# Performance work log

Hardware: AMD Instinct MI355X
Metric: run time of the kernel (lower is better)

Reference implementation:

```python
import jax, jax.numpy as jnp
import numpy as np

D = 1024      # d_model
H = 16        # query heads
KV = 4        # kv heads
HD = D // H   # head dim = 64
REP = H // KV
E = 16        # experts
K = 2         # experts per token
INTER = 1408  # moe intermediate size
EPS = 1e-6
B, S = 2, 1024


def rmsnorm(x, w):
    return x * jax.lax.rsqrt(jnp.mean(x * x, axis=-1, keepdims=True) + EPS) * w


def rotate_half(x):
    x1, x2 = jnp.split(x, 2, axis=-1)
    return jnp.concatenate([-x2, x1], axis=-1)


def setup_inputs() -> dict:
    key = jax.random.key(0)
    ks = jax.random.split(key, 12)
    x = jax.random.normal(ks[0], (B, S, D), jnp.float32)
    # RoPE tables [S, HD]
    inv = 1.0 / (10000.0 ** (np.arange(0, HD, 2, dtype=np.float64) / HD))
    ang = np.arange(S, dtype=np.float64)[:, None] * inv[None, :]
    ang = np.concatenate([ang, ang], axis=1)
    cos = jnp.asarray(np.cos(ang), jnp.float32)
    sin = jnp.asarray(np.sin(ang), jnp.float32)
    w = lambda k, shape: jax.random.normal(k, shape, jnp.float32) * 0.02
    return dict(
        x=x, cos=cos, sin=sin,
        ln1_w=jnp.ones((D,), jnp.float32),
        wq=w(ks[1], (D, H * HD)),
        wk=w(ks[2], (D, KV * HD)),
        wv=w(ks[3], (D, KV * HD)),
        wo=w(ks[4], (H * HD, D)),
        qn_w=jnp.ones((HD,), jnp.float32),
        kn_w=jnp.ones((HD,), jnp.float32),
        ln2_w=jnp.ones((D,), jnp.float32),
        router_w=w(ks[5], (D, E)),
        w_gate=w(ks[6], (E, D, INTER)),
        w_up=w(ks[7], (E, D, INTER)),
        w_down=w(ks[8], (E, INTER, D)),
    )


def reference(x, cos, sin, ln1_w, wq, wk, wv, wo, qn_w, kn_w, ln2_w,
              router_w, w_gate, w_up, w_down):
    b, s, _ = x.shape
    # --- GQA attention with qk RMSNorm + RoPE, causal ---
    h = rmsnorm(x, ln1_w)
    q = (h @ wq).reshape(b, s, H, HD)
    k = (h @ wk).reshape(b, s, KV, HD)
    v = (h @ wv).reshape(b, s, KV, HD)
    q = rmsnorm(q, qn_w)
    k = rmsnorm(k, kn_w)
    c = cos[None, :, None, :]
    sn = sin[None, :, None, :]
    q = q * c + rotate_half(q) * sn
    k = k * c + rotate_half(k) * sn
    k = jnp.repeat(k, REP, axis=2)  # [b,s,H,HD]
    v = jnp.repeat(v, REP, axis=2)
    scores = jnp.einsum('bqhd,bkhd->bhqk', q, k) / jnp.sqrt(jnp.float32(HD))
    causal = jnp.tril(jnp.ones((s, s), bool))
    scores = jnp.where(causal[None, None], scores, jnp.finfo(scores.dtype).min)
    p = jax.nn.softmax(scores, axis=-1)
    attn = jnp.einsum('bhqk,bkhd->bqhd', p, v).reshape(b, s, H * HD) @ wo
    x = x + attn
    # --- Sparse MoE FFN (top-k softmax router, normalized top-k probs, SwiGLU experts) ---
    t = rmsnorm(x, ln2_w).reshape(b * s, D)
    logits = t @ router_w                       # [T,E]
    probs = jax.nn.softmax(logits, axis=-1)
    top_v, top_i = jax.lax.top_k(probs, K)      # [T,K]
    top_v = top_v / jnp.sum(top_v, axis=-1, keepdims=True)
    onehot = jax.nn.one_hot(top_i, E, dtype=t.dtype)      # [T,K,E]
    w_dense = jnp.einsum('tke,tk->te', onehot, top_v)     # [T,E] combine weights
    g = jnp.einsum('td,edi->eti', t, w_gate)
    u = jnp.einsum('td,edi->eti', t, w_up)
    eo = jnp.einsum('eti,eid->etd', jax.nn.silu(g) * u, w_down)
    moe = jnp.einsum('te,etd->td', w_dense, eo).reshape(b, s, D)
    # load-balancing aux loss: E * sum_e f_e * P_e
    f = jnp.mean(onehot, axis=(0, 1))           # fraction of assignments per expert
    aux = jnp.float32(E) * jnp.sum(f * jnp.mean(probs, axis=0))
    return x + moe, aux
```

## Files before the change

kernel.cpp:

```cpp
#include <hip/hip_runtime.h>

#define BB 2
#define SS 1024
#define DD 1024
#define HH 16
#define KVH 4
#define HDD 64
#define EE 16
#define II 1408
#define TT (BB*SS)
#define EPS_ 1e-6f

typedef unsigned short u16;
typedef __bf16 bf16x8 __attribute__((ext_vector_type(8)));
typedef _Float16 f16x8 __attribute__((ext_vector_type(8)));
typedef float f32x4 __attribute__((ext_vector_type(4)));

__device__ __forceinline__ float wred_sum(float v) {
#pragma unroll
  for (int o = 32; o > 0; o >>= 1) v += __shfl_xor(v, o);
  return v;
}

__device__ __forceinline__ u16 f2b(float f) {
  __bf16 h = (__bf16)f;
  return __builtin_bit_cast(u16, h);
}

__device__ __forceinline__ bf16x8 ld_frag(const u16* p) {
  return __builtin_bit_cast(bf16x8, *(const uint4*)p);
}
__device__ __forceinline__ f16x8 ldh(const u16* p) {
  return __builtin_bit_cast(f16x8, *(const uint4*)p);
}

__device__ __forceinline__ void split2h(float v, u16* o0, u16* o1) {
  _Float16 a = (_Float16)v;
  float fa = (float)a;
  _Float16 b = (_Float16)((v - fa) * 2048.0f);
  *o0 = __builtin_bit_cast(u16, a);
  *o1 = __builtin_bit_cast(u16, b);
}

#define CVAL(fm, nf, r) (accm[fm][nf][r] + accx[fm][nf][r] * 4.8828125e-4f)

__global__ __launch_bounds__(256) void k_rmsnorm_split2(const float* __restrict__ x,
    const float* __restrict__ w, u16* __restrict__ o0, u16* __restrict__ o1) {
  int row = blockIdx.x, tid = threadIdx.x;
  float4 v = ((const float4*)(x + (size_t)row * DD))[tid];
  float ss = v.x*v.x + v.y*v.y + v.z*v.z + v.w*v.w;
  ss = wred_sum(ss);
  __shared__ float red[4];
  if ((tid & 63) == 0) red[tid >> 6] = ss;
  __syncthreads();
  float tot = red[0] + red[1] + red[2] + red[3];
  float sc = rsqrtf(tot * (1.0f / DD) + EPS_);
  float4 wv = ((const float4*)w)[tid];
  float vals[4] = {v.x*sc*wv.x, v.y*sc*wv.y, v.z*sc*wv.z, v.w*sc*wv.w};
  ushort4 s0, s1;
  split2h(vals[0], &s0.x, &s1.x);
  split2h(vals[1], &s0.y, &s1.y);
  split2h(vals[2], &s0.z, &s1.z);
  split2h(vals[3], &s0.w, &s1.w);
  size_t base = (size_t)row * DD + tid * 4;
  *(ushort4*)&o0[base] = s0;
  *(ushort4*)&o1[base] = s1;
}

__global__ __launch_bounds__(256) void k_transpose_split2(const float* __restrict__ Wm,
    u16* __restrict__ T0, u16* __restrict__ T1, int K, int N) {
  int n0 = blockIdx.x * 64, k0 = blockIdx.y * 64;
  __shared__ float tile[64][65];
  int tc = threadIdx.x & 15, tr = threadIdx.x >> 4;
#pragma unroll
  for (int kk = 0; kk < 64; kk += 16) {
    float4 v = *(const float4*)&Wm[(size_t)(k0 + kk + tr) * N + n0 + tc * 4];
    tile[kk + tr][tc*4+0] = v.x; tile[kk + tr][tc*4+1] = v.y;
    tile[kk + tr][tc*4+2] = v.z; tile[kk + tr][tc*4+3] = v.w;
  }
  __syncthreads();
#pragma unroll
  for (int nn = 0; nn < 64; nn += 16) {
    int n = nn + tr;
    ushort4 s0, s1;
    split2h(tile[tc*4+0][n], &s0.x, &s1.x);
    split2h(tile[tc*4+1][n], &s0.y, &s1.y);
    split2h(tile[tc*4+2][n], &s0.z, &s1.z);
    split2h(tile[tc*4+3][n], &s0.w, &s1.w);
    size_t base = (size_t)(n0 + n) * K + k0 + tc * 4;
    *(ushort4*)&T0[base] = s0;
    *(ushort4*)&T1[base] = s1;
  }
}

#define S2GEMM_BODY(a0p, a1p, b0p, b1p, KTOT) \
  __shared__ __align__(16) u16 A0s[128][56], A1s[128][56]; \
  __shared__ __align__(16) u16 B0s[64][56], B1s[64][56]; \
  int tid = threadIdx.x, lane = tid & 63, w = tid >> 6; \
  int wm = (w & 1) * 64, wn = (w >> 1) * 32; \
  int lr = lane & 15, lk = (lane >> 4) * 8; \
  int br = tid >> 2, bc = (tid & 3) * 8; \
  f32x4 accm[4][2] = {}, accx[4][2] = {}; \
  for (int k0 = 0; k0 < (KTOT); k0 += 32) { \
    uint4 a0v0 = *(const uint4*)((a0p) + (size_t)br * (KTOT) + k0 + bc); \
    uint4 a0v1 = *(const uint4*)((a0p) + (size_t)(64 + br) * (KTOT) + k0 + bc); \
    uint4 a1v0 = *(const uint4*)((a1p) + (size_t)br * (KTOT) + k0 + bc); \
    uint4 a1v1 = *(const uint4*)((a1p) + (size_t)(64 + br) * (KTOT) + k0 + bc); \
    uint4 b0v = *(const uint4*)((b0p) + (size_t)br * (KTOT) + k0 + bc); \
    uint4 b1v = *(const uint4*)((b1p) + (size_t)br * (KTOT) + k0 + bc); \
    __syncthreads(); \
    *(uint4*)&A0s[br][bc] = a0v0; \
    *(uint4*)&A0s[64 + br][bc] = a0v1; \
    *(uint4*)&A1s[br][bc] = a1v0; \
    *(uint4*)&A1s[64 + br][bc] = a1v1; \
    *(uint4*)&B0s[br][bc] = b0v; \
    *(uint4*)&B1s[br][bc] = b1v; \
    __syncthreads(); \
    f16x8 bq0[2], bq1[2]; \
    _Pragma("unroll") \
    for (int nf = 0; nf < 2; ++nf) { \
      bq0[nf] = ldh(&B0s[wn + nf*16 + lr][lk]); \
      bq1[nf] = ldh(&B1s[wn + nf*16 + lr][lk]); } \
    _Pragma("unroll") \
    for (int fm = 0; fm < 4; ++fm) { \
      f16x8 a0 = ldh(&A0s[wm + fm*16 + lr][lk]); \
      f16x8 a1 = ldh(&A1s[wm + fm*16 + lr][lk]); \
      _Pragma("unroll") \
      for (int nf = 0; nf < 2; ++nf) { \
        accm[fm][nf] = __builtin_amdgcn_mfma_f32_16x16x32_f16(a0, bq0[nf], accm[fm][nf], 0, 0, 0); \
        f32x4 cx = accx[fm][nf]; \
        cx = __builtin_amdgcn_mfma_f32_16x16x32_f16(a0, bq1[nf], cx, 0, 0, 0); \
        cx = __builtin_amdgcn_mfma_f32_16x16x32_f16(a1, bq0[nf], cx, 0, 0, 0); \
        accx[fm][nf] = cx; } } \
  }

__global__ __launch_bounds__(256) void k_qkv_s2(
    const u16* __restrict__ h0, const u16* __restrict__ h1,
    const u16* __restrict__ wqt0, const u16* __restrict__ wqt1,
    const u16* __restrict__ wkt0, const u16* __restrict__ wkt1,
    const u16* __restrict__ wvt0, const u16* __restrict__ wvt1,
    float* __restrict__ qb, float* __restrict__ kb, float* __restrict__ vb) {
  int nt = blockIdx.x, m0 = blockIdx.y * 128;
  const u16 *B0, *B1; float* Cm; int Nm, n0;
  if (nt < 16)      { B0 = wqt0; B1 = wqt1; Cm = qb; Nm = 1024; n0 = nt * 64; }
  else if (nt < 20) { B0 = wkt0; B1 = wkt1; Cm = kb; Nm = 256;  n0 = (nt - 16) * 64; }
  else              { B0 = wvt0; B1 = wvt1; Cm = vb; Nm = 256;  n0 = (nt - 20) * 64; }
  const u16* a0p = h0 + (size_t)m0 * 1024;
  const u16* a1p = h1 + (size_t)m0 * 1024;
  const u16* b0p = B0 + (size_t)n0 * 1024;
  const u16* b1p = B1 + (size_t)n0 * 1024;
  S2GEMM_BODY(a0p, a1p, b0p, b1p, 1024)
#pragma unroll
  for (int fm = 0; fm < 4; ++fm)
#pragma unroll
    for (int nf = 0; nf < 2; ++nf)
#pragma unroll
      for (int r = 0; r < 4; ++r) {
        int row = m0 + wm + fm*16 + (lane >> 4) * 4 + r;
        Cm[(size_t)row * Nm + n0 + wn + nf*16 + lr] = CVAL(fm, nf, r);
      }
}

__global__ __launch_bounds__(256) void k_qknorm_rope_split2(
    const float* __restrict__ qb, const float* __restrict__ kb,
    const float* __restrict__ qnw, const float* __restrict__ knw,
    const float* __restrict__ cosb, const float* __restrict__ sinb,
    u16* __restrict__ q0a, u16* __restrict__ q1a,
    u16* __restrict__ k0a, u16* __restrict__ k1a) {
  int tok = blockIdx.x, grp = blockIdx.y;
  int wv = threadIdx.x >> 6, d = threadIdx.x & 63;
  int s = tok & (SS - 1);
  const float* ptr; const float* wn;
  if (grp < 4) { ptr = qb + (size_t)tok * 1024 + (grp * 4 + wv) * 64; wn = qnw; }
  else         { ptr = kb + (size_t)tok * 256 + wv * 64;              wn = knw; }
  float v = ptr[d];
  float ssum = wred_sum(v * v);
  float rms = rsqrtf(ssum * (1.0f / 64.0f) + EPS_);
  float nv = v * rms * wn[d];
  float pn = __shfl_xor(nv, 32);
  float rot = (d < 32) ? -pn : pn;
  float val = nv * cosb[s * 64 + d] + rot * sinb[s * 64 + d];
  u16 a, b;
  split2h(val, &a, &b);
  if (grp < 4) {
    size_t idx = (size_t)tok * 1024 + (grp * 4 + wv) * 64 + d;
    q0a[idx] = a; q1a[idx] = b;
  } else {
    size_t idx = (size_t)tok * 256 + wv * 64 + d;
    k0a[idx] = a; k1a[idx] = b;
  }
}

__global__ __launch_bounds__(256) void k_splitv2(const float* __restrict__ vb,
    u16* __restrict__ t0, u16* __restrict__ t1) {
  int k0 = blockIdx.x * 64, bkv = blockIdx.y;
  int b = bkv >> 2, kv = bkv & 3;
  __shared__ float tile[64][65];
  int tc = threadIdx.x & 15, tr = threadIdx.x >> 4;
#pragma unroll
  for (int kk = 0; kk < 64; kk += 16) {
    float4 v = *(const float4*)&vb[(size_t)(b * 1024 + k0 + kk + tr) * 256 + kv * 64 + tc * 4];
    tile[kk + tr][tc*4+0] = v.x; tile[kk + tr][tc*4+1] = v.y;
    tile[kk + tr][tc*4+2] = v.z; tile[kk + tr][tc*4+3] = v.w;
  }
  __syncthreads();
#pragma unroll
  for (int dd = 0; dd < 64; dd += 16) {
    int d = dd + tr;
    ushort4 s0, s1;
    split2h(tile[tc*4+0][d], &s0.x, &s1.x);
    split2h(tile[tc*4+1][d], &s0.y, &s1.y);
    split2h(tile[tc*4+2][d], &s0.z, &s1.z);
    split2h(tile[tc*4+3][d], &s0.w, &s1.w);
    size_t base = (size_t)(bkv * 64 + d) * 1024 + k0 + tc * 4;
    *(ushort4*)&t0[base] = s0;
    *(ushort4*)&t1[base] = s1;
  }
}

__global__ __launch_bounds__(256) void k_flash(
    const u16* __restrict__ qs0, const u16* __restrict__ qs1,
    const u16* __restrict__ ks0, const u16* __restrict__ ks1,
    const u16* __restrict__ vt0, const u16* __restrict__ vt1,
    u16* __restrict__ at0, u16* __restrict__ at1) {
  int pair = blockIdx.x, bh = blockIdx.y;
  int b = bh >> 4, hh = bh & 15, kv = hh >> 2;
  int bkv = b * 4 + kv;
  __shared__ __align__(16) u16 Qs0[64*72], Qs1[64*72];
  __shared__ __align__(16) u16 Ks0[64*72], Ks1[64*72];
  __shared__ __align__(16) u16 Vs0[64*72], Vs1[64*72];
  __shared__ __align__(16) u16 Ps0[64*72], Ps1[64*72];
  int tid = threadIdx.x, lane = tid & 63, w = tid >> 6;
  int lr = lane & 15, g = lane >> 4;
  int wq0 = w * 16;
  const float c2 = 4.8828125e-4f;
#pragma unroll 1
  for (int half = 0; half < 2; ++half) {
    int qt = (half == 0) ? pair : (15 - pair);
    int q0 = qt * 64;
#pragma unroll
    for (int i = 0; i < 2; ++i) {
      int idx = tid + i * 256, r = idx >> 3, c = (idx & 7) * 8;
      size_t off = (size_t)(b * 1024 + q0 + r) * 1024 + hh * 64 + c;
      *(uint4*)&Qs0[r*72 + c] = *(const uint4*)(qs0 + off);
      *(uint4*)&Qs1[r*72 + c] = *(const uint4*)(qs1 + off);
    }
    f32x4 Om[4] = {}, Ox[4] = {};
    float mrow[4] = {-3.4e38f, -3.4e38f, -3.4e38f, -3.4e38f};
    float lrow[4] = {};
    __syncthreads();
    for (int kt = 0; kt <= qt; ++kt) {
      int k0 = kt * 64;
#pragma unroll
      for (int i = 0; i < 2; ++i) {
        int idx = tid + i * 256, r = idx >> 3, c = (idx & 7) * 8;
        size_t koff = (size_t)(b * 1024 + k0 + r) * 256 + kv * 64 + c;
        *(uint4*)&Ks0[r*72 + c] = *(const uint4*)(ks0 + koff);
        *(uint4*)&Ks1[r*72 + c] = *(const uint4*)(ks1 + koff);
        size_t voff = (size_t)(bkv * 64 + r) * 1024 + k0 + c;
        *(uint4*)&Vs0[r*72 + c] = *(const uint4*)(vt0 + voff);
        *(uint4*)&Vs1[r*72 + c] = *(const uint4*)(vt1 + voff);
      }
      __syncthreads();
      f32x4 Sm[4] = {}, Sx[4] = {};
#pragma unroll
      for (int ks = 0; ks < 2; ++ks) {
        f16x8 a0 = ldh(&Qs0[(wq0 + lr)*72 + ks*32 + g*8]);
        f16x8 a1 = ldh(&Qs1[(wq0 + lr)*72 + ks*32 + g*8]);
#pragma unroll
        for (int nt = 0; nt < 4; ++nt) {
          f16x8 b0 = ldh(&Ks0[(nt*16 + lr)*72 + ks*32 + g*8]);
          f16x8 b1 = ldh(&Ks1[(nt*16 + lr)*72 + ks*32 + g*8]);
          Sm[nt] = __builtin_amdgcn_mfma_f32_16x16x32_f16(a0, b0, Sm[nt], 0, 0, 0);
          f32x4 cx = Sx[nt];
          cx = __builtin_amdgcn_mfma_f32_16x16x32_f16(a0, b1, cx, 0, 0, 0);
          cx = __builtin_amdgcn_mfma_f32_16x16x32_f16(a1, b0, cx, 0, 0, 0);
          Sx[nt] = cx;
        }
      }
      bool diag = (kt == qt);
      float pvv[4][4], scl[4];
#pragma unroll
      for (int r = 0; r < 4; ++r) {
        int rowloc = wq0 + g*4 + r;
        float rm = -3.4e38f;
#pragma unroll
        for (int nt = 0; nt < 4; ++nt) {
          float s = (Sm[nt][r] + Sx[nt][r] * c2) * 0.125f;
          bool valid = (!diag) || (nt*16 + lr <= rowloc);
          s = valid ? s : -3.4e38f;
          pvv[r][nt] = s;
          rm = fmaxf(rm, s);
        }
#pragma unroll
        for (int o = 1; o < 16; o <<= 1) rm = fmaxf(rm, __shfl_xor(rm, o));
        float mn = fmaxf(mrow[r], rm);
        scl[r] = __expf(mrow[r] - mn);
        mrow[r] = mn;
        float rs = 0.f;
#pragma unroll
        for (int nt = 0; nt < 4; ++nt) {
          float p = (pvv[r][nt] > -3.0e38f) ? __expf(pvv[r][nt] - mn) : 0.f;
          pvv[r][nt] = p;
          rs += p;
        }
#pragma unroll
        for (int o = 1; o < 16; o <<= 1) rs += __shfl_xor(rs, o);
        lrow[r] = lrow[r] * scl[r] + rs;
      }
#pragma unroll
      for (int nt = 0; nt < 4; ++nt)
#pragma unroll
        for (int r = 0; r < 4; ++r) { Om[nt][r] *= scl[r]; Ox[nt][r] *= scl[r]; }
#pragma unroll
      for (int r = 0; r < 4; ++r)
#pragma unroll
        for (int nt = 0; nt < 4; ++nt) {
          u16 pa, pb;
          split2h(pvv[r][nt], &pa, &pb);
          int addr = (wq0 + g*4 + r)*72 + nt*16 + lr;
          Ps0[addr] = pa; Ps1[addr] = pb;
        }
#pragma unroll
      for (int ks = 0; ks < 2; ++ks) {
        f16x8 p0 = ldh(&Ps0[(wq0 + lr)*72 + ks*32 + g*8]);
        f16x8 p1 = ldh(&Ps1[(wq0 + lr)*72 + ks*32 + g*8]);
#pragma unroll
        for (int nt = 0; nt < 4; ++nt) {
          f16x8 v0 = ldh(&Vs0[(nt*16 + lr)*72 + ks*32 + g*8]);
          f16x8 v1 = ldh(&Vs1[(nt*16 + lr)*72 + ks*32 + g*8]);
          Om[nt] = __builtin_amdgcn_mfma_f32_16x16x32_f16(p0, v0, Om[nt], 0, 0, 0);
          f32x4 cx = Ox[nt];
          cx = __builtin_amdgcn_mfma_f32_16x16x32_f16(p0, v1, cx, 0, 0, 0);
          cx = __builtin_amdgcn_mfma_f32_16x16x32_f16(p1, v0, cx, 0, 0, 0);
          Ox[nt] = cx;
        }
      }
      __syncthreads();
    }
#pragma unroll
    for (int nt = 0; nt < 4; ++nt)
#pragma unroll
      for (int r = 0; r < 4; ++r) {
        float val = (Om[nt][r] + Ox[nt][r] * c2) / lrow[r];
        u16 sa, sb;
        split2h(val, &sa, &sb);
        size_t idx = (size_t)(b * 1024 + q0 + wq0 + g*4 + r) * 1024 + hh * 64 + nt*16 + lr;
        at0[idx] = sa; at1[idx] = sb;
      }
    __syncthreads();
  }
}

__global__ __launch_bounds__(256) void k_wo_s2(
    const u16* __restrict__ at0, const u16* __restrict__ at1,
    const u16* __restrict__ wot0, const u16* __restrict__ wot1,
    const float* __restrict__ x, float* __restrict__ x2) {
  int n0 = blockIdx.x * 64, m0 = blockIdx.y * 128;
  const u16* a0p = at0 + (size_t)m0 * 1024;
  const u16* a1p = at1 + (size_t)m0 * 1024;
  const u16* b0p = wot0 + (size_t)n0 * 1024;
  const u16* b1p = wot1 + (size_t)n0 * 1024;
  S2GEMM_BODY(a0p, a1p, b0p, b1p, 1024)
#pragma unroll
  for (int fm = 0; fm < 4; ++fm)
#pragma unroll
    for (int nf = 0; nf < 2; ++nf)
#pragma unroll
      for (int r = 0; r < 4; ++r) {
        int row = m0 + wm + fm*16 + (lane >> 4) * 4 + r;
        int col = n0 + wn + nf*16 + lr;
        x2[(size_t)row * 1024 + col] = CVAL(fm, nf, r) + x[(size_t)row * 1024 + col];
      }
}

__global__ __launch_bounds__(256) void k_rmsnorm_logits(const float* __restrict__ x2,
    const float* __restrict__ w, const float* __restrict__ rw,
    u16* __restrict__ tbh, float* __restrict__ logits) {
  int row = blockIdx.x, tid = threadIdx.x;
  __shared__ __align__(16) float tl[1024];
  __shared__ float part[16][16];
  __shared__ float red[4];
  float4 v = ((const float4*)(x2 + (size_t)row * DD))[tid];
  float ss = v.x*v.x + v.y*v.y + v.z*v.z + v.w*v.w;
  ss = wred_sum(ss);
  if ((tid & 63) == 0) red[tid >> 6] = ss;
  __syncthreads();
  float tot = red[0] + red[1] + red[2] + red[3];
  float sc = rsqrtf(tot * (1.0f / DD) + EPS_);
  float4 wv = ((const float4*)w)[tid];
  float4 o = make_float4(v.x*sc*wv.x, v.y*sc*wv.y, v.z*sc*wv.z, v.w*sc*wv.w);
  ((float4*)tl)[tid] = o;
  ushort4 hb = make_ushort4(f2b(o.x), f2b(o.y), f2b(o.z), f2b(o.w));
  *(ushort4*)&tbh[(size_t)row * DD + tid * 4] = hb;
  __syncthreads();
  int e = tid & 15, ch = tid >> 4;
  float p = 0.f;
#pragma unroll 8
  for (int j = 0; j < 64; ++j) p = fmaf(tl[ch * 64 + j], rw[(ch * 64 + j) * EE + e], p);
  part[ch][e] = p;
  __syncthreads();
  if (tid < 16) {
    float s = 0.f;
#pragma unroll
    for (int c = 0; c < 16; ++c) s += part[c][tid];
    logits[(size_t)row * EE + tid] = s;
  }
}

__global__ __launch_bounds__(256) void k_route(const float* __restrict__ logits,
    int* __restrict__ cnt, int* __restrict__ listTok, int* __restrict__ tokslot,
    float* __restrict__ topw, float* __restrict__ psum) {
  int tid = threadIdx.x;
  int tok = blockIdx.x * 256 + tid;
  __shared__ int lcnt[16], gbase[16];
  __shared__ float lps[16];
  if (tid < 16) { lcnt[tid] = 0; lps[tid] = 0.f; }
  __syncthreads();
  float pr[16];
#pragma unroll
  for (int g = 0; g < 4; ++g) {
    float4 v = *(const float4*)&logits[(size_t)tok * EE + g * 4];
    pr[g*4+0] = v.x; pr[g*4+1] = v.y; pr[g*4+2] = v.z; pr[g*4+3] = v.w;
  }
  float mx = pr[0];
#pragma unroll
  for (int i = 1; i < 16; ++i) mx = fmaxf(mx, pr[i]);
  float s = 0.f;
#pragma unroll
  for (int i = 0; i < 16; ++i) { pr[i] = __expf(pr[i] - mx); s += pr[i]; }
  float inv = 1.0f / s;
#pragma unroll
  for (int i = 0; i < 16; ++i) pr[i] *= inv;
  int i1 = 0; float v1 = pr[0];
#pragma unroll
  for (int i = 1; i < 16; ++i) if (pr[i] > v1) { v1 = pr[i]; i1 = i; }
  int i2 = -1; float v2 = -1.f;
#pragma unroll
  for (int i = 0; i < 16; ++i) if (i != i1 && pr[i] > v2) { v2 = pr[i]; i2 = i; }
  float wsum = v1 + v2;
  int lp1 = atomicAdd(&lcnt[i1], 1);
  int lp2 = atomicAdd(&lcnt[i2], 1);
#pragma unroll
  for (int e = 0; e < 16; ++e) {
    float v = wred_sum(pr[e]);
    if ((tid & 63) == 0) atomicAdd(&lps[e], v);
  }
  __syncthreads();
  if (tid < 16) {
    gbase[tid] = atomicAdd(&cnt[tid], lcnt[tid]);
    atomicAdd(&psum[tid], lps[tid]);
  }
  __syncthreads();
  int p1 = gbase[i1] + lp1, p2 = gbase[i2] + lp2;
  listTok[i1 * 2048 + p1] = tok;
  listTok[i2 * 2048 + p2] = tok;
  tokslot[tok * 2 + 0] = i1 * 2048 + p1;
  tokslot[tok * 2 + 1] = i2 * 2048 + p2;
  topw[tok * 2 + 0] = v1 / wsum;
  topw[tok * 2 + 1] = v2 / wsum;
}

__global__ void k_zero(int* cnt, float* psum) {
  int t = threadIdx.x;
  if (t < 16) { cnt[t] = 0; psum[t] = 0.f; }
}

__global__ void k_prefix(const int* __restrict__ cnt, int* __restrict__ offs) {
  if (threadIdx.x == 0) {
    int s = 0;
    for (int e = 0; e < 16; ++e) { offs[e] = s; s += cnt[e]; }
  }
}

__global__ __launch_bounds__(256) void k_gu_mfma(const u16* __restrict__ tbh,
    const float* __restrict__ wg, const float* __restrict__ wu,
    const int* __restrict__ cnt, const int* __restrict__ offs,
    const int* __restrict__ listTok, u16* __restrict__ act) {
  int e = blockIdx.z;
  int ce = cnt[e];
  int m0 = blockIdx.y * 128;
  if (m0 >= ce) return;
  int n0 = blockIdx.x * 64;
  __shared__ __align__(16) u16 Ah[128][56];
  __shared__ __align__(16) u16 Gh[64][56];
  __shared__ __align__(16) u16 Uh[64][56];
  __shared__ int rows[128];
  int tid = threadIdx.x;
  if (tid < 128) {
    int m = m0 + tid;
    rows[tid] = listTok[e * 2048 + (m < ce ? m : ce - 1)];
  }
  __syncthreads();
  int s_arow = tid >> 1, s_acol = (tid & 1) * 16;
  int s_nc = (tid & 31) * 2, s_kg = (tid >> 5) * 4;
  const float* wge = wg + (size_t)e * DD * II + n0;
  const float* wue = wu + (size_t)e * DD * II + n0;
  const u16* ap = tbh + (size_t)rows[s_arow] * DD + s_acol;
  int lane = tid & 63, w = tid >> 6;
  int wm = (w & 1) * 64, wn = (w >> 1) * 32;
  int lr = lane & 15, lk = (lane >> 4) * 8;
  f32x4 accg[4][2] = {};
  f32x4 accu[4][2] = {};
  for (int k0 = 0; k0 < DD; k0 += 32) {
    uint4 av0 = *(const uint4*)(ap + k0);
    uint4 av1 = *(const uint4*)(ap + k0 + 8);
    float2 g0 = *(const float2*)&wge[(size_t)(k0 + s_kg + 0) * II + s_nc];
    float2 g1 = *(const float2*)&wge[(size_t)(k0 + s_kg + 1) * II + s_nc];
    float2 g2 = *(const float2*)&wge[(size_t)(k0 + s_kg + 2) * II + s_nc];
    float2 g3 = *(const float2*)&wge[(size_t)(k0 + s_kg + 3) * II + s_nc];
    float2 u0 = *(const float2*)&wue[(size_t)(k0 + s_kg + 0) * II + s_nc];
    float2 u1 = *(const float2*)&wue[(size_t)(k0 + s_kg + 1) * II + s_nc];
    float2 u2 = *(const float2*)&wue[(size_t)(k0 + s_kg + 2) * II + s_nc];
    float2 u3 = *(const float2*)&wue[(size_t)(k0 + s_kg + 3) * II + s_nc];
    *(uint4*)&Ah[s_arow][s_acol]     = av0;
    *(uint4*)&Ah[s_arow][s_acol + 8] = av1;
    *(ushort4*)&Gh[s_nc][s_kg]     = make_ushort4(f2b(g0.x), f2b(g1.x), f2b(g2.x), f2b(g3.x));
    *(ushort4*)&Gh[s_nc + 1][s_kg] = make_ushort4(f2b(g0.y), f2b(g1.y), f2b(g2.y), f2b(g3.y));
    *(ushort4*)&Uh[s_nc][s_kg]     = make_ushort4(f2b(u0.x), f2b(u1.x), f2b(u2.x), f2b(u3.x));
    *(ushort4*)&Uh[s_nc + 1][s_kg] = make_ushort4(f2b(u0.y), f2b(u1.y), f2b(u2.y), f2b(u3.y));
    __syncthreads();
    bf16x8 af[4];
#pragma unroll
    for (int fm = 0; fm < 4; ++fm) af[fm] = ld_frag(&Ah[wm + fm*16 + lr][lk]);
#pragma unroll
    for (int nf = 0; nf < 2; ++nf) {
      bf16x8 bg = ld_frag(&Gh[wn + nf*16 + lr][lk]);
      bf16x8 bu = ld_frag(&Uh[wn + nf*16 + lr][lk]);
#pragma unroll
      for (int fm = 0; fm < 4; ++fm) {
        accg[fm][nf] = __builtin_amdgcn_mfma_f32_16x16x32_bf16(af[fm], bg, accg[fm][nf], 0, 0, 0);
        accu[fm][nf] = __builtin_amdgcn_mfma_f32_16x16x32_bf16(af[fm], bu, accu[fm][nf], 0, 0, 0);
      }
    }
    __syncthreads();
  }
  int ob = offs[e];
#pragma unroll
  for (int fm = 0; fm < 4; ++fm)
#pragma unroll
    for (int nf = 0; nf < 2; ++nf)
#pragma unroll
      for (int r = 0; r < 4; ++r) {
        int m = m0 + wm + fm*16 + (lane >> 4) * 4 + r;
        if (m < ce) {
          float g = accg[fm][nf][r], u = accu[fm][nf][r];
          float sv = (g / (1.f + __expf(-g))) * u;
          act[(size_t)(ob + m) * II + n0 + wn + nf*16 + (lane & 15)] = f2b(sv);
        }
      }
}

__global__ __launch_bounds__(256) void k_down_mfma(const u16* __restrict__ act,
    const float* __restrict__ wd, const int* __restrict__ cnt, const int* __restrict__ offs,
    float* __restrict__ eo) {
  int e = blockIdx.z;
  int ce = cnt[e];
  int m0 = blockIdx.y * 128;
  if (m0 >= ce) return;
  int n0 = blockIdx.x * 64;
  __shared__ __align__(16) u16 Ah[128][56];
  __shared__ __align__(16) u16 Bh[64][56];
  int tid = threadIdx.x;
  int ob = offs[e];
  int s_arow = tid >> 1, s_acol = (tid & 1) * 16;
  int s_nc = (tid & 31) * 2, s_kg = (tid >> 5) * 4;
  int mrow = m0 + s_arow; if (mrow >= ce) mrow = ce - 1;
  const u16* ap = act + (size_t)(ob + mrow) * II + s_acol;
  const float* wde = wd + (size_t)e * II * DD + n0;
  int lane = tid & 63, w = tid >> 6;
  int wm = (w & 1) * 64, wn = (w >> 1) * 32;
  int lr = lane & 15, lk = (lane >> 4) * 8;
  f32x4 acc[4][2] = {};
  for (int k0 = 0; k0 < II; k0 += 32) {
    uint4 av0 = *(const uint4*)(ap + k0);
    uint4 av1 = *(const uint4*)(ap + k0 + 8);
    float2 b0 = *(const float2*)&wde[(size_t)(k0 + s_kg + 0) * DD + s_nc];
    float2 b1 = *(const float2*)&wde[(size_t)(k0 + s_kg + 1) * DD + s_nc];
    float2 b2 = *(const float2*)&wde[(size_t)(k0 + s_kg + 2) * DD + s_nc];
    float2 b3 = *(const float2*)&wde[(size_t)(k0 + s_kg + 3) * DD + s_nc];
    *(uint4*)&Ah[s_arow][s_acol]     = av0;
    *(uint4*)&Ah[s_arow][s_acol + 8] = av1;
    *(ushort4*)&Bh[s_nc][s_kg]     = make_ushort4(f2b(b0.x), f2b(b1.x), f2b(b2.x), f2b(b3.x));
    *(ushort4*)&Bh[s_nc + 1][s_kg] = make_ushort4(f2b(b0.y), f2b(b1.y), f2b(b2.y), f2b(b3.y));
    __syncthreads();
    bf16x8 af[4];
#pragma unroll
    for (int fm = 0; fm < 4; ++fm) af[fm] = ld_frag(&Ah[wm + fm*16 + lr][lk]);
#pragma unroll
    for (int nf = 0; nf < 2; ++nf) {
      bf16x8 bb = ld_frag(&Bh[wn + nf*16 + lr][lk]);
#pragma unroll
      for (int fm = 0; fm < 4; ++fm)
        acc[fm][nf] = __builtin_amdgcn_mfma_f32_16x16x32_bf16(af[fm], bb, acc[fm][nf], 0, 0, 0);
    }
    __syncthreads();
  }
#pragma unroll
  for (int fm = 0; fm < 4; ++fm)
#pragma unroll
    for (int nf = 0; nf < 2; ++nf)
#pragma unroll
      for (int r = 0; r < 4; ++r) {
        int m = m0 + wm + fm*16 + (lane >> 4) * 4 + r;
        if (m < ce)
          eo[(size_t)(ob + m) * DD + n0 + wn + nf*16 + (lane & 15)] = acc[fm][nf][r];
      }
}

__global__ __launch_bounds__(256) void k_final(const float* __restrict__ x2,
    const float* __restrict__ eo, const int* __restrict__ tokslot,
    const float* __restrict__ topw, const int* __restrict__ offs, float* __restrict__ out) {
  int tok = blockIdx.x, tid = threadIdx.x;
  int c0 = tokslot[tok * 2], c1 = tokslot[tok * 2 + 1];
  int s0 = offs[c0 >> 11] + (c0 & 2047);
  int s1 = offs[c1 >> 11] + (c1 & 2047);
  float w0 = topw[tok * 2], w1 = topw[tok * 2 + 1];
  float4 a = ((const float4*)(x2 + (size_t)tok * DD))[tid];
  float4 e0 = ((const float4*)(eo + (size_t)s0 * DD))[tid];
  float4 e1 = ((const float4*)(eo + (size_t)s1 * DD))[tid];
  float4 o = make_float4(a.x + w0*e0.x + w1*e1.x, a.y + w0*e0.y + w1*e1.y,
                         a.z + w0*e0.z + w1*e1.z, a.w + w0*e0.w + w1*e1.w);
  ((float4*)(out + (size_t)tok * DD))[tid] = o;
}

__global__ void k_aux(const int* __restrict__ cnt, const float* __restrict__ psum,
                      float* __restrict__ out) {
  if (threadIdx.x == 0) {
    float a = 0.f;
    for (int e = 0; e < 16; ++e)
      a += ((float)cnt[e] * (1.0f / 4096.0f)) * (psum[e] * (1.0f / 2048.0f));
    out[(size_t)TT * DD] = 16.0f * a;
  }
}

extern "C" void kernel_launch(void* const* d_in, const int* in_sizes, int n_in,
                              void* d_out, int out_size, void* d_ws, size_t ws_size,
                              hipStream_t stream) {
  const float* x    = (const float*)d_in[0];
  const float* cosb = (const float*)d_in[1];
  const float* sinb = (const float*)d_in[2];
  const float* ln1w = (const float*)d_in[3];
  const float* wq   = (const float*)d_in[4];
  const float* wk   = (const float*)d_in[5];
  const float* wv   = (const float*)d_in[6];
  const float* wo   = (const float*)d_in[7];
  const float* qnw  = (const float*)d_in[8];
  const float* knw  = (const float*)d_in[9];
  const float* ln2w = (const float*)d_in[10];
  const float* rw   = (const float*)d_in[11];
  const float* wg   = (const float*)d_in[12];
  const float* wu   = (const float*)d_in[13];
  const float* wd   = (const float*)d_in[14];
  float* out = (float*)d_out;

  float* W = (float*)d_ws;
  int*   cnt     = (int*)W;
  int*   offs    = (int*)(W + 16);
  float* psum    = W + 32;
  int*   tokslot = (int*)(W + 64);
  float* topw    = W + 4160;
  int*   listTok = (int*)(W + 8256);
  float* logits  = W + 41024;
  size_t o = 81920;
#define ALLOC_F(name, n)   float* name = W + o; o += (n);
#define ALLOC_U16(name, n) u16* name = (u16*)(W + o); o += ((size_t)(n) + 1) / 2;
  ALLOC_U16(h0, 2097152) ALLOC_U16(h1, 2097152)
  ALLOC_F(qb, 2097152) ALLOC_F(kb, 524288) ALLOC_F(vb, 524288)
  ALLOC_U16(wqt0, 1048576) ALLOC_U16(wqt1, 1048576)
  ALLOC_U16(wkt0, 262144) ALLOC_U16(wkt1, 262144)
  ALLOC_U16(wvt0, 262144) ALLOC_U16(wvt1, 262144)
  ALLOC_U16(wot0, 1048576) ALLOC_U16(wot1, 1048576)
  ALLOC_U16(qs0, 2097152) ALLOC_U16(qs1, 2097152)
  ALLOC_U16(ks0, 524288) ALLOC_U16(ks1, 524288)
  ALLOC_U16(vt0, 524288) ALLOC_U16(vt1, 524288)
  ALLOC_U16(at0, 2097152) ALLOC_U16(at1, 2097152)
  ALLOC_F(x2, 2097152)
  ALLOC_U16(tbh, 2097152)
  ALLOC_U16(act, 5767168)
  ALLOC_F(eo, 4194304)
#undef ALLOC_F
#undef ALLOC_U16

  k_zero<<<1, 64, 0, stream>>>(cnt, psum);
  k_rmsnorm_split2<<<TT, 256, 0, stream>>>(x, ln1w, h0, h1);
  k_transpose_split2<<<dim3(16, 16), 256, 0, stream>>>(wq, wqt0, wqt1, 1024, 1024);
  k_transpose_split2<<<dim3(4, 16), 256, 0, stream>>>(wk, wkt0, wkt1, 1024, 256);
  k_transpose_split2<<<dim3(4, 16), 256, 0, stream>>>(wv, wvt0, wvt1, 1024, 256);
  k_transpose_split2<<<dim3(16, 16), 256, 0, stream>>>(wo, wot0, wot1, 1024, 1024);
  k_qkv_s2<<<dim3(24, 16), 256, 0, stream>>>(h0, h1,
      wqt0, wqt1, wkt0, wkt1, wvt0, wvt1, qb, kb, vb);
  k_qknorm_rope_split2<<<dim3(TT, 5), 256, 0, stream>>>(qb, kb, qnw, knw, cosb, sinb,
      qs0, qs1, ks0, ks1);
  k_splitv2<<<dim3(16, 8), 256, 0, stream>>>(vb, vt0, vt1);
  k_flash<<<dim3(8, 32), 256, 0, stream>>>(qs0, qs1, ks0, ks1, vt0, vt1, at0, at1);
  k_wo_s2<<<dim3(16, 16), 256, 0, stream>>>(at0, at1, wot0, wot1, x, x2);
  k_rmsnorm_logits<<<TT, 256, 0, stream>>>(x2, ln2w, rw, tbh, logits);
  k_route<<<TT / 256, 256, 0, stream>>>(logits, cnt, listTok, tokslot, topw, psum);
  k_prefix<<<1, 1, 0, stream>>>(cnt, offs);
  k_gu_mfma<<<dim3(22, 16, 16), 256, 0, stream>>>(tbh, wg, wu, cnt, offs, listTok, act);
  k_down_mfma<<<dim3(16, 16, 16), 256, 0, stream>>>(act, wd, cnt, offs, eo);
  k_final<<<TT, 256, 0, stream>>>(x2, eo, tokslot, topw, offs, out);
  k_aux<<<1, 1, 0, stream>>>(cnt, psum, out);
}
```

Measured before the change: 388.6 us.

## Split flash blocks per query tile and widen expert weight loads to float4

The flash attention kernel now launches one block per query tile, ordered longest-first, instead of pairing two tiles per block. This doubles the grid from 256 to 512 blocks to improve occupancy and load balance on the GPU. The MoE gate/up and down kernels now load fp32 weights as float4 per thread. In gate/up, each half of the block fetches one of the two matrices; in down, only half the threads load weights. The aim is fewer, wider global loads, at the cost of more LDS store work per thread and idle lanes during the down-proj weight loads.

```diff
diff --git a/kernel.cpp b/kernel.cpp
--- a/kernel.cpp
+++ b/kernel.cpp
@@ -223,7 +223,7 @@
     const u16* __restrict__ ks0, const u16* __restrict__ ks1,
     const u16* __restrict__ vt0, const u16* __restrict__ vt1,
     u16* __restrict__ at0, u16* __restrict__ at1) {
-  int pair = blockIdx.x, bh = blockIdx.y;
+  int qt = 15 - blockIdx.x, bh = blockIdx.y;
   int b = bh >> 4, hh = bh & 15, kv = hh >> 2;
   int bkv = b * 4 + kv;
   __shared__ __align__(16) u16 Qs0[64*72], Qs1[64*72];
@@ -234,122 +234,117 @@
   int lr = lane & 15, g = lane >> 4;
   int wq0 = w * 16;
   const float c2 = 4.8828125e-4f;
-#pragma unroll 1
-  for (int half = 0; half < 2; ++half) {
-    int qt = (half == 0) ? pair : (15 - pair);
-    int q0 = qt * 64;
+  int q0 = qt * 64;
+#pragma unroll
+  for (int i = 0; i < 2; ++i) {
+    int idx = tid + i * 256, r = idx >> 3, c = (idx & 7) * 8;
+    size_t off = (size_t)(b * 1024 + q0 + r) * 1024 + hh * 64 + c;
+    *(uint4*)&Qs0[r*72 + c] = *(const uint4*)(qs0 + off);
+    *(uint4*)&Qs1[r*72 + c] = *(const uint4*)(qs1 + off);
+  }
+  f32x4 Om[4] = {}, Ox[4] = {};
+  float mrow[4] = {-3.4e38f, -3.4e38f, -3.4e38f, -3.4e38f};
+  float lrow[4] = {};
+  __syncthreads();
+  for (int kt = 0; kt <= qt; ++kt) {
+    int k0 = kt * 64;
 #pragma unroll
     for (int i = 0; i < 2; ++i) {
       int idx = tid + i * 256, r = idx >> 3, c = (idx & 7) * 8;
-      size_t off = (size_t)(b * 1024 + q0 + r) * 1024 + hh * 64 + c;
-      *(uint4*)&Qs0[r*72 + c] = *(const uint4*)(qs0 + off);
-      *(uint4*)&Qs1[r*72 + c] = *(const uint4*)(qs1 + off);
-    }
-    f32x4 Om[4] = {}, Ox[4] = {};
-    float mrow[4] = {-3.4e38f, -3.4e38f, -3.4e38f, -3.4e38f};
-    float lrow[4] = {};
+      size_t koff = (size_t)(b * 1024 + k0 + r) * 256 + kv * 64 + c;
+      *(uint4*)&Ks0[r*72 + c] = *(const uint4*)(ks0 + koff);
+      *(uint4*)&Ks1[r*72 + c] = *(const uint4*)(ks1 + koff);
+      size_t voff = (size_t)(bkv * 64 + r) * 1024 + k0 + c;
+      *(uint4*)&Vs0[r*72 + c] = *(const uint4*)(vt0 + voff);
+      *(uint4*)&Vs1[r*72 + c] = *(const uint4*)(vt1 + voff);
+    }
     __syncthreads();
-    for (int kt = 0; kt <= qt; ++kt) {
-      int k0 = kt * 64;
-#pragma unroll
-      for (int i = 0; i < 2; ++i) {
-        int idx = tid + i * 256, r = idx >> 3, c = (idx & 7) * 8;
-        size_t koff = (size_t)(b * 1024 + k0 + r) * 256 + kv * 64 + c;
-        *(uint4*)&Ks0[r*72 + c] = *(const uint4*)(ks0 + koff);
-        *(uint4*)&Ks1[r*72 + c] = *(const uint4*)(ks1 + koff);
-        size_t voff = (size_t)(bkv * 64 + r) * 1024 + k0 + c;
-        *(uint4*)&Vs0[r*72 + c] = *(const uint4*)(vt0 + voff);
-        *(uint4*)&Vs1[r*72 + c] = *(const uint4*)(vt1 + voff);
-      }
-      __syncthreads();
-      f32x4 Sm[4] = {}, Sx[4] = {};
-#pragma unroll
-      for (int ks = 0; ks < 2; ++ks) {
-        f16x8 a0 = ldh(&Qs0[(wq0 + lr)*72 + ks*32 + g*8]);
-        f16x8 a1 = ldh(&Qs1[(wq0 + lr)*72 + ks*32 + g*8]);
-#pragma unroll
-        for (int nt = 0; nt < 4; ++nt) {
-          f16x8 b0 = ldh(&Ks0[(nt*16 + lr)*72 + ks*32 + g*8]);
-          f16x8 b1 = ldh(&Ks1[(nt*16 + lr)*72 + ks*32 + g*8]);
-          Sm[nt] = __builtin_amdgcn_mfma_f32_16x16x32_f16(a0, b0, Sm[nt], 0, 0, 0);
-          f32x4 cx = Sx[nt];
-          cx = __builtin_amdgcn_mfma_f32_16x16x32_f16(a0, b1, cx, 0, 0, 0);
-          cx = __builtin_amdgcn_mfma_f32_16x16x32_f16(a1, b0, cx, 0, 0, 0);
-          Sx[nt] = cx;
-        }
-      }
-      bool diag = (kt == qt);
-      float pvv[4][4], scl[4];
-#pragma unroll
-      for (int r = 0; r < 4; ++r) {
-        int rowloc = wq0 + g*4 + r;
-        float rm = -3.4e38f;
-#pragma unroll
-        for (int nt = 0; nt < 4; ++nt) {
-          float s = (Sm[nt][r] + Sx[nt][r] * c2) * 0.125f;
-          bool valid = (!diag) || (nt*16 + lr <= rowloc);
-          s = valid ? s : -3.4e38f;
-          pvv[r][nt] = s;
-          rm = fmaxf(rm, s);
-        }
-#pragma unroll
-        for (int o = 1; o < 16; o <<= 1) rm = fmaxf(rm, __shfl_xor(rm, o));
-        float mn = fmaxf(mrow[r], rm);
-        scl[r] = __expf(mrow[r] - mn);
-        mrow[r] = mn;
-        float rs = 0.f;
-#pragma unroll
-        for (int nt = 0; nt < 4; ++nt) {
-          float p = (pvv[r][nt] > -3.0e38f) ? __expf(pvv[r][nt] - mn) : 0.f;
-          pvv[r][nt] = p;
-          rs += p;
-        }
-#pragma unroll
-        for (int o = 1; o < 16; o <<= 1) rs += __shfl_xor(rs, o);
-        lrow[r] = lrow[r] * scl[r] + rs;
-      }
-#pragma unroll
-      for (int nt = 0; nt < 4; ++nt)
-#pragma unroll
-        for (int r = 0; r < 4; ++r) { Om[nt][r] *= scl[r]; Ox[nt][r] *= scl[r]; }
-#pragma unroll
-      for (int r = 0; r < 4; ++r)
-#pragma unroll
-        for (int nt = 0; nt < 4; ++nt) {
-          u16 pa, pb;
-          split2h(pvv[r][nt], &pa, &pb);
-          int addr = (wq0 + g*4 + r)*72 + nt*16 + lr;
-          Ps0[addr] = pa; Ps1[addr] = pb;
-        }
-#pragma unroll
-      for (int ks = 0; ks < 2; ++ks) {
-        f16x8 p0 = ldh(&Ps0[(wq0 + lr)*72 + ks*32 + g*8]);
-        f16x8 p1 = ldh(&Ps1[(wq0 + lr)*72 + ks*32 + g*8]);
-#pragma unroll
-        for (int nt = 0; nt < 4; ++nt) {
-          f16x8 v0 = ldh(&Vs0[(nt*16 + lr)*72 + ks*32 + g*8]);
-          f16x8 v1 = ldh(&Vs1[(nt*16 + lr)*72 + ks*32 + g*8]);
-          Om[nt] = __builtin_amdgcn_mfma_f32_16x16x32_f16(p0, v0, Om[nt], 0, 0, 0);
-          f32x4 cx = Ox[nt];
-          cx = __builtin_amdgcn_mfma_f32_16x16x32_f16(p0, v1, cx, 0, 0, 0);
-          cx = __builtin_amdgcn_mfma_f32_16x16x32_f16(p1, v0, cx, 0, 0, 0);
-          Ox[nt] = cx;
-        }
-      }
-      __syncthreads();
+    f32x4 Sm[4] = {}, Sx[4] = {};
+#pragma unroll
+    for (int ks = 0; ks < 2; ++ks) {
+      f16x8 a0 = ldh(&Qs0[(wq0 + lr)*72 + ks*32 + g*8]);
+      f16x8 a1 = ldh(&Qs1[(wq0 + lr)*72 + ks*32 + g*8]);
+#pragma unroll
+      for (int nt = 0; nt < 4; ++nt) {
+        f16x8 b0 = ldh(&Ks0[(nt*16 + lr)*72 + ks*32 + g*8]);
+        f16x8 b1 = ldh(&Ks1[(nt*16 + lr)*72 + ks*32 + g*8]);
+        Sm[nt] = __builtin_amdgcn_mfma_f32_16x16x32_f16(a0, b0, Sm[nt], 0, 0, 0);
+        f32x4 cx = Sx[nt];
+        cx = __builtin_amdgcn_mfma_f32_16x16x32_f16(a0, b1, cx, 0, 0, 0);
+        cx = __builtin_amdgcn_mfma_f32_16x16x32_f16(a1, b0, cx, 0, 0, 0);
+        Sx[nt] = cx;
+      }
+    }
+    bool diag = (kt == qt);
+    float pvv[4][4], scl[4];
+#pragma unroll
+    for (int r = 0; r < 4; ++r) {
+      int rowloc = wq0 + g*4 + r;
+      float rm = -3.4e38f;
+#pragma unroll
+      for (int nt = 0; nt < 4; ++nt) {
+        float s = (Sm[nt][r] + Sx[nt][r] * c2) * 0.125f;
+        bool valid = (!diag) || (nt*16 + lr <= rowloc);
+        s = valid ? s : -3.4e38f;
+        pvv[r][nt] = s;
+        rm = fmaxf(rm, s);
+      }
+#pragma unroll
+      for (int o = 1; o < 16; o <<= 1) rm = fmaxf(rm, __shfl_xor(rm, o));
+      float mn = fmaxf(mrow[r], rm);
+      scl[r] = __expf(mrow[r] - mn);
+      mrow[r] = mn;
+      float rs = 0.f;
+#pragma unroll
+      for (int nt = 0; nt < 4; ++nt) {
+        float p = (pvv[r][nt] > -3.0e38f) ? __expf(pvv[r][nt] - mn) : 0.f;
+        pvv[r][nt] = p;
+        rs += p;
+      }
+#pragma unroll
+      for (int o = 1; o < 16; o <<= 1) rs += __shfl_xor(rs, o);
+      lrow[r] = lrow[r] * scl[r] + rs;
     }
 #pragma unroll
     for (int nt = 0; nt < 4; ++nt)
 #pragma unroll
-      for (int r = 0; r < 4; ++r) {
-        float val = (Om[nt][r] + Ox[nt][r] * c2) / lrow[r];
-        u16 sa, sb;
-        split2h(val, &sa, &sb);
-        size_t idx = (size_t)(b * 1024 + q0 + wq0 + g*4 + r) * 1024 + hh * 64 + nt*16 + lr;
-        at0[idx] = sa; at1[idx] = sb;
-      }
+      for (int r = 0; r < 4; ++r) { Om[nt][r] *= scl[r]; Ox[nt][r] *= scl[r]; }
+#pragma unroll
+    for (int r = 0; r < 4; ++r)
+#pragma unroll
+      for (int nt = 0; nt < 4; ++nt) {
+        u16 pa, pb;
+        split2h(pvv[r][nt], &pa, &pb);
+        int addr = (wq0 + g*4 + r)*72 + nt*16 + lr;
+        Ps0[addr] = pa; Ps1[addr] = pb;
+      }
+#pragma unroll
+    for (int ks = 0; ks < 2; ++ks) {
+      f16x8 p0 = ldh(&Ps0[(wq0 + lr)*72 + ks*32 + g*8]);
+      f16x8 p1 = ldh(&Ps1[(wq0 + lr)*72 + ks*32 + g*8]);
+#pragma unroll
+      for (int nt = 0; nt < 4; ++nt) {
+        f16x8 v0 = ldh(&Vs0[(nt*16 + lr)*72 + ks*32 + g*8]);
+        f16x8 v1 = ldh(&Vs1[(nt*16 + lr)*72 + ks*32 + g*8]);
+        Om[nt] = __builtin_amdgcn_mfma_f32_16x16x32_f16(p0, v0, Om[nt], 0, 0, 0);
+        f32x4 cx = Ox[nt];
+        cx = __builtin_amdgcn_mfma_f32_16x16x32_f16(p0, v1, cx, 0, 0, 0);
+        cx = __builtin_amdgcn_mfma_f32_16x16x32_f16(p1, v0, cx, 0, 0, 0);
+        Ox[nt] = cx;
+      }
+    }
     __syncthreads();
   }
+#pragma unroll
+  for (int nt = 0; nt < 4; ++nt)
+#pragma unroll
+    for (int r = 0; r < 4; ++r) {
+      float val = (Om[nt][r] + Ox[nt][r] * c2) / lrow[r];
+      u16 sa, sb;
+      split2h(val, &sa, &sb);
+      size_t idx = (size_t)(b * 1024 + q0 + wq0 + g*4 + r) * 1024 + hh * 64 + nt*16 + lr;
+      at0[idx] = sa; at1[idx] = sb;
+    }
 }
 
 __global__ __launch_bounds__(256) void k_wo_s2(
@@ -493,9 +488,12 @@
   }
   __syncthreads();
   int s_arow = tid >> 1, s_acol = (tid & 1) * 16;
-  int s_nc = (tid & 31) * 2, s_kg = (tid >> 5) * 4;
+  int wsel = tid >> 7, t = tid & 127;
+  int s_n4 = (t & 15) * 4, s_kg = (t >> 4) * 4;
   const float* wge = wg + (size_t)e * DD * II + n0;
   const float* wue = wu + (size_t)e * DD * II + n0;
+  const float* wsrc = wsel ? wue : wge;
+  u16* Wdst = wsel ? &Uh[0][0] : &Gh[0][0];
   const u16* ap = tbh + (size_t)rows[s_arow] * DD + s_acol;
   int lane = tid & 63, w = tid >> 6;
   int wm = (w & 1) * 64, wn = (w >> 1) * 32;
@@ -505,20 +503,16 @@
   for (int k0 = 0; k0 < DD; k0 += 32) {
     uint4 av0 = *(const uint4*)(ap + k0);
     uint4 av1 = *(const uint4*)(ap + k0 + 8);
-    float2 g0 = *(const float2*)&wge[(size_t)(k0 + s_kg + 0) * II + s_nc];
-    float2 g1 = *(const float2*)&wge[(size_t)(k0 + s_kg + 1) * II + s_nc];
-    float2 g2 = *(const float2*)&wge[(size_t)(k0 + s_kg + 2) * II + s_nc];
-    float2 g3 = *(const float2*)&wge[(size_t)(k0 + s_kg + 3) * II + s_nc];
-    float2 u0 = *(const float2*)&wue[(size_t)(k0 + s_kg + 0) * II + s_nc];
-    float2 u1 = *(const float2*)&wue[(size_t)(k0 + s_kg + 1) * II + s_nc];
-    float2 u2 = *(const float2*)&wue[(size_t)(k0 + s_kg + 2) * II + s_nc];
-    float2 u3 = *(const float2*)&wue[(size_t)(k0 + s_kg + 3) * II + s_nc];
+    float4 r0 = *(const float4*)&wsrc[(size_t)(k0 + s_kg + 0) * II + s_n4];
+    float4 r1 = *(const float4*)&wsrc[(size_t)(k0 + s_kg + 1) * II + s_n4];
+    float4 r2 = *(const float4*)&wsrc[(size_t)(k0 + s_kg + 2) * II + s_n4];
+    float4 r3 = *(const float4*)&wsrc[(size_t)(k0 + s_kg + 3) * II + s_n4];
     *(uint4*)&Ah[s_arow][s_acol]     = av0;
     *(uint4*)&Ah[s_arow][s_acol + 8] = av1;
-    *(ushort4*)&Gh[s_nc][s_kg]     = make_ushort4(f2b(g0.x), f2b(g1.x), f2b(g2.x), f2b(g3.x));
-    *(ushort4*)&Gh[s_nc + 1][s_kg] = make_ushort4(f2b(g0.y), f2b(g1.y), f2b(g2.y), f2b(g3.y));
-    *(ushort4*)&Uh[s_nc][s_kg]     = make_ushort4(f2b(u0.x), f2b(u1.x), f2b(u2.x), f2b(u3.x));
-    *(ushort4*)&Uh[s_nc + 1][s_kg] = make_ushort4(f2b(u0.y), f2b(u1.y), f2b(u2.y), f2b(u3.y));
+    *(ushort4*)&Wdst[(s_n4+0)*56 + s_kg] = make_ushort4(f2b(r0.x), f2b(r1.x), f2b(r2.x), f2b(r3.x));
+    *(ushort4*)&Wdst[(s_n4+1)*56 + s_kg] = make_ushort4(f2b(r0.y), f2b(r1.y), f2b(r2.y), f2b(r3.y));
+    *(ushort4*)&Wdst[(s_n4+2)*56 + s_kg] = make_ushort4(f2b(r0.z), f2b(r1.z), f2b(r2.z), f2b(r3.z));
+    *(ushort4*)&Wdst[(s_n4+3)*56 + s_kg] = make_ushort4(f2b(r0.w), f2b(r1.w), f2b(r2.w), f2b(r3.w));
     __syncthreads();
     bf16x8 af[4];
 #pragma unroll
@@ -564,7 +558,8 @@
   int tid = threadIdx.x;
   int ob = offs[e];
   int s_arow = tid >> 1, s_acol = (tid & 1) * 16;
-  int s_nc = (tid & 31) * 2, s_kg = (tid >> 5) * 4;
+  int t = tid & 127;
+  int s_n4 = (t & 15) * 4, s_kg = (t >> 4) * 4;
   int mrow = m0 + s_arow; if (mrow >= ce) mrow = ce - 1;
   const u16* ap = act + (size_t)(ob + mrow) * II + s_acol;
   const float* wde = wd + (size_t)e * II * DD + n0;
@@ -575,14 +570,21 @@
   for (int k0 = 0; k0 < II; k0 += 32) {
     uint4 av0 = *(const uint4*)(ap + k0);
     uint4 av1 = *(const uint4*)(ap + k0 + 8);
-    float2 b0 = *(const float2*)&wde[(size_t)(k0 + s_kg + 0) * DD + s_nc];
-    float2 b1 = *(const float2*)&wde[(size_t)(k0 + s_kg + 1) * DD + s_nc];
-    float2 b2 = *(const float2*)&wde[(size_t)(k0 + s_kg + 2) * DD + s_nc];
-    float2 b3 = *(const float2*)&wde[(size_t)(k0 + s_kg + 3) * DD + s_nc];
+    float4 r0, r1, r2, r3;
+    if (tid < 128) {
+      r0 = *(const float4*)&wde[(size_t)(k0 + s_kg + 0) * DD + s_n4];
+      r1 = *(const float4*)&wde[(size_t)(k0 + s_kg + 1) * DD + s_n4];
+      r2 = *(const float4*)&wde[(size_t)(k0 + s_kg + 2) * DD + s_n4];
+      r3 = *(const float4*)&wde[(size_t)(k0 + s_kg + 3) * DD + s_n4];
+    }
     *(uint4*)&Ah[s_arow][s_acol]     = av0;
     *(uint4*)&Ah[s_arow][s_acol + 8] = av1;
-    *(ushort4*)&Bh[s_nc][s_kg]     = make_ushort4(f2b(b0.x), f2b(b1.x), f2b(b2.x), f2b(b3.x));
-    *(ushort4*)&Bh[s_nc + 1][s_kg] = make_ushort4(f2b(b0.y), f2b(b1.y), f2b(b2.y), f2b(b3.y));
+    if (tid < 128) {
+      *(ushort4*)&Bh[s_n4+0][s_kg] = make_ushort4(f2b(r0.x), f2b(r1.x), f2b(r2.x), f2b(r3.x));
+      *(ushort4*)&Bh[s_n4+1][s_kg] = make_ushort4(f2b(r0.y), f2b(r1.y), f2b(r2.y), f2b(r3.y));
+      *(ushort4*)&Bh[s_n4+2][s_kg] = make_ushort4(f2b(r0.z), f2b(r1.z), f2b(r2.z), f2b(r3.z));
+      *(ushort4*)&Bh[s_n4+3][s_kg] = make_ushort4(f2b(r0.w), f2b(r1.w), f2b(r2.w), f2b(r3.w));
+    }
     __syncthreads();
     bf16x8 af[4];
 #pragma unroll
@@ -693,7 +695,7 @@
   k_qknorm_rope_split2<<<dim3(TT, 5), 256, 0, stream>>>(qb, kb, qnw, knw, cosb, sinb,
       qs0, qs1, ks0, ks1);
   k_splitv2<<<dim3(16, 8), 256, 0, stream>>>(vb, vt0, vt1);
-  k_flash<<<dim3(8, 32), 256, 0, stream>>>(qs0, qs1, ks0, ks1, vt0, vt1, at0, at1);
+  k_flash<<<dim3(16, 32), 256, 0, stream>>>(qs0, qs1, ks0, ks1, vt0, vt1, at0, at1);
   k_wo_s2<<<dim3(16, 16), 256, 0, stream>>>(at0, at1, wot0, wot1, x, x2);
   k_rmsnorm_logits<<<TT, 256, 0, stream>>>(x2, ln2w, rw, tbh, logits);
   k_route<<<TT / 256, 256, 0, stream>>>(logits, cnt, listTok, tokslot, topw, psum);
```

Result: slower. 404.8 us (+4.2%).
